# Kernel optimization log

Measured on AMD Instinct MI355X. Metric: run time of the kernel, lower is better.

## Reference

```python
import jax, jax.numpy as jnp
import numpy as np

D_MODEL = 1024
NUM_HEADS = 16
HEAD_DIM = D_MODEL // NUM_HEADS


def setup_inputs() -> dict:
    key = jax.random.key(0)
    ks = jax.random.split(key, 8)
    B, S = 4, 1024
    scale = 1.0 / np.sqrt(D_MODEL)
    return {
        "x": jax.random.normal(ks[0], (B, S, D_MODEL), jnp.float32),
        "tokens": jax.random.normal(ks[1], (B, 1, D_MODEL), jnp.float32),
        "Wq": jax.random.normal(ks[2], (D_MODEL, D_MODEL), jnp.float32) * scale,
        "bq": jnp.zeros((D_MODEL,), jnp.float32),
        "Wk": jax.random.normal(ks[3], (D_MODEL, D_MODEL), jnp.float32) * scale,
        "bk": jnp.zeros((D_MODEL,), jnp.float32),
        "Wv": jax.random.normal(ks[4], (D_MODEL, D_MODEL), jnp.float32) * scale,
        "bv": jnp.zeros((D_MODEL,), jnp.float32),
    }


def _split_heads(t):
    # [B, S, D] -> [B, H, S, hd]
    B, S, _ = t.shape
    return t.reshape(B, S, NUM_HEADS, HEAD_DIM).transpose(0, 2, 1, 3)


def reference(x, tokens, Wq, bq, Wk, bk, Wv, bv):
    # Projections (torch Linear: y = x @ W.T + b)
    Q = _split_heads(x @ Wq.T + bq)          # [B,H,S,hd]
    K = _split_heads(x @ Wk.T + bk)
    V = _split_heads(x @ Wv.T + bv)
    tQ = _split_heads(tokens @ Wq.T + bq)    # [B,H,1,hd] -> broadcast
    tK = _split_heads(tokens @ Wk.T + bk)
    cQ = Q + tQ
    cK = K + tK
    scores = jnp.einsum("bhqd,bhkd->bhqk", cQ, cK) / jnp.sqrt(jnp.float32(HEAD_DIM))
    attn = jax.nn.softmax(scores, axis=-1)
    out = jnp.einsum("bhqk,bhkd->bhqd", attn, V)  # [B,H,S,hd]
    B, H, S, hd = out.shape
    return out.transpose(0, 2, 1, 3).reshape(B, S, D_MODEL)
```

## Files before the change

kernel.cpp:

```cpp
#include <hip/hip_runtime.h>
#include <hip/hip_bf16.h>


typedef __bf16 bf16;
typedef __bf16 bf16x8 __attribute__((ext_vector_type(8)));
typedef float  f32x4  __attribute__((ext_vector_type(4)));

#define LOG2E 1.4426950408889634f

__device__ __forceinline__ void gll16(const void* g, void* l) {
  __builtin_amdgcn_global_load_lds(
      (const __attribute__((address_space(1))) unsigned int*)g,
      (__attribute__((address_space(3))) unsigned int*)l, 16, 0, 0);
}

__device__ __forceinline__ unsigned cvtpk(float a, float b) {
  unsigned r;
  asm("v_cvt_pk_bf16_f32 %0, %1, %2" : "=v"(r) : "v"(a), "v"(b));
  return r;
}

__global__ void prep_kernel(const float* __restrict__ x, const float* __restrict__ tok,
                            const float* __restrict__ wq, const float* __restrict__ wk,
                            const float* __restrict__ wv,
                            bf16* __restrict__ xb, bf16* __restrict__ xt,
                            bf16* __restrict__ wdst) {
  const int bid = blockIdx.x;
  if (bid < 2048) {
    const size_t e = ((size_t)bid * 256 + threadIdx.x) * 8;
    const int b = (int)(e >> 20);
    const int d = (int)(e & 1023);
    const float4 a0 = *(const float4*)(x + e);
    const float4 a1 = *(const float4*)(x + e + 4);
    const float4 t0 = *(const float4*)(tok + b * 1024 + d);
    const float4 t1 = *(const float4*)(tok + b * 1024 + d + 4);
    bf16x8 vb, vt;
    vb[0]=(bf16)a0.x; vb[1]=(bf16)a0.y; vb[2]=(bf16)a0.z; vb[3]=(bf16)a0.w;
    vb[4]=(bf16)a1.x; vb[5]=(bf16)a1.y; vb[6]=(bf16)a1.z; vb[7]=(bf16)a1.w;
    vt[0]=(bf16)(a0.x+t0.x); vt[1]=(bf16)(a0.y+t0.y); vt[2]=(bf16)(a0.z+t0.z); vt[3]=(bf16)(a0.w+t0.w);
    vt[4]=(bf16)(a1.x+t1.x); vt[5]=(bf16)(a1.y+t1.y); vt[6]=(bf16)(a1.z+t1.z); vt[7]=(bf16)(a1.w+t1.w);
    *(bf16x8*)(xb + e) = vb;
    *(bf16x8*)(xt + e) = vt;
  } else {
    const size_t e = ((size_t)(bid - 2048) * 256 + threadIdx.x) * 8;
    const float* src; size_t off;
    if (e < (size_t)(1u<<20))      { src = wq; off = e; }
    else if (e < (size_t)(2u<<20)) { src = wk; off = e - (1u<<20); }
    else                           { src = wv; off = e - (2u<<20); }
    const float4 a0 = *(const float4*)(src + off);
    const float4 a1 = *(const float4*)(src + off + 4);
    bf16x8 v;
    v[0]=(bf16)a0.x; v[1]=(bf16)a0.y; v[2]=(bf16)a0.z; v[3]=(bf16)a0.w;
    v[4]=(bf16)a1.x; v[5]=(bf16)a1.y; v[6]=(bf16)a1.z; v[7]=(bf16)a1.w;
    *(bf16x8*)(wdst + e) = v;
  }
}

__global__ __launch_bounds__(256, 3) void qkv_gemm_kernel(
    const bf16* __restrict__ xt, const bf16* __restrict__ xb,
    const bf16* __restrict__ wq, const bf16* __restrict__ wk, const bf16* __restrict__ wv,
    const float* __restrict__ bq, const float* __restrict__ bk, const float* __restrict__ bv,
    bf16* __restrict__ cq, bf16* __restrict__ ck, bf16* __restrict__ vt)
{
  __shared__ __align__(16) char LDSG[49152];
  char* As = LDSG;
  char* Bs = LDSG + 24576;
  const int t = threadIdx.x, w = t >> 6, l = t & 63, g = l >> 4, c = l & 15;
  const int wr = w >> 1, wc = w & 1;
  const int wgid = blockIdx.x;
  const int xcd = wgid & 7;
  const int p = wgid >> 3;
  const int z = p >> 5;
  const int q = p & 31;
  const bf16 *A, *B; const float* bias; bf16* outp;
  int tm, tn;
  if (z < 2) { tm = xcd * 4 + (q & 3); tn = q >> 2; }
  else       { tm = q >> 2; tn = xcd * 4 + (q & 3); }
  if (z == 0)      { A = xt; B = wq; bias = bq; outp = cq; }
  else if (z == 1) { A = xt; B = wk; bias = bk; outp = ck; }
  else             { A = wv; B = xb; bias = bv; outp = vt; }
  const int m0 = tm * 128, n0 = tn * 128;

  f32x4 acc[4][4] = {};

  const int u = (t & 7) ^ ((t >> 3) & 7);
  const size_t ssw = (size_t)(2 * (t >> 3) + (u >> 2)) * 2048 + (size_t)(u & 3) * 16;
  const char* aga = (const char*)A + (size_t)m0 * 2048 + ssw;
  const char* bga = (const char*)B + (size_t)n0 * 2048 + ssw;

#define GSTAGE(slot, kt)                                                 \
  {                                                                      \
    const size_t ko = (size_t)(kt) * 64;            \
    char* ad = As + (slot) * 8192 + t * 16;                              \
    char* bd = Bs + (slot) * 8192 + t * 16;                              \
    gll16(aga + ko,          ad);                                        \
    gll16(aga + ko + 131072, ad + 4096);             \
    gll16(bga + ko,          bd);                                        \
    gll16(bga + ko + 131072, bd + 4096);                                 \
  }

  GSTAGE(0, 0);
  GSTAGE(1, 1);
  int st = 2;
  int s  = 0;
  for (int kt = 0; kt < 32; ++kt) {
    if (kt < 30) {
      GSTAGE(st, kt + 2);
      asm volatile("s_waitcnt vmcnt(8)" ::: "memory");
    } else if (kt == 30) {
      asm volatile("s_waitcnt vmcnt(4)" ::: "memory");
    } else {
      asm volatile("s_waitcnt vmcnt(0)" ::: "memory");
    }
    __builtin_amdgcn_sched_barrier(0);
    __builtin_amdgcn_s_barrier();

    const char* Ab = As + s * 8192;
    const char* Bb = Bs + s * 8192;
    bf16x8 af[4], bfr[4];
#pragma unroll
    for (int mf = 0; mf < 4; ++mf) {
      const int mrow = wr * 64 + mf * 16 + c;
      af[mf] = *(const bf16x8*)(Ab + (mrow >> 1) * 128 +
                                (((((mrow & 1) << 2) + g) ^ ((mrow >> 1) & 7)) << 4));
    }
#pragma unroll
    for (int nf = 0; nf < 4; ++nf) {
      const int nrow = wc * 64 + nf * 16 + c;
      bfr[nf] = *(const bf16x8*)(Bb + (nrow >> 1) * 128 +
                                 (((((nrow & 1) << 2) + g) ^ ((nrow >> 1) & 7)) << 4));
    }
    __builtin_amdgcn_s_setprio(1);
#pragma unroll
    for (int mf = 0; mf < 4; ++mf)
#pragma unroll
      for (int nf = 0; nf < 4; ++nf)
        acc[mf][nf] = __builtin_amdgcn_mfma_f32_16x16x32_bf16(af[mf], bfr[nf], acc[mf][nf], 0, 0, 0);
    __builtin_amdgcn_s_setprio(0);
    __builtin_amdgcn_s_barrier();
    s  = (s  == 2) ? 0 : s + 1;
    st = (st == 2) ? 0 : st + 1;
  }
#undef GSTAGE

  if (z < 2) {
    const float sc = (z == 0) ? 0.125f * LOG2E : 1.0f;
#pragma unroll
    for (int mf = 0; mf < 4; ++mf)
#pragma unroll
      for (int nf = 0; nf < 4; ++nf) {
        const int n = n0 + wc * 64 + nf * 16 + c;
        const int h = n >> 6, d = n & 63;
        const float bsum = 2.0f * bias[n];
#pragma unroll
        for (int r = 0; r < 4; ++r) {
          const int m = m0 + wr * 64 + mf * 16 + g * 4 + r;
          const int b = m >> 10, s2 = m & 1023;
          outp[(((size_t)(b * 16 + h)) * 1024 + s2) * 64 + d] = (bf16)((acc[mf][nf][r] + bsum) * sc);
        }
      }
  } else {
#pragma unroll
    for (int mf = 0; mf < 4; ++mf)
#pragma unroll
      for (int nf = 0; nf < 4; ++nf) {
        const int n = n0 + wc * 64 + nf * 16 + c;
        const int b = n >> 10, s2 = n & 1023;
#pragma unroll
        for (int r = 0; r < 4; ++r) {
          const int m = m0 + wr * 64 + mf * 16 + g * 4 + r;
          const int h = m >> 6, d = m & 63;
          outp[(((size_t)(b * 16 + h)) * 64 + d) * 1024 + s2] = (bf16)(acc[mf][nf][r] + bias[m]);
        }
      }
  }
}

__global__ __launch_bounds__(256) void attn_kernel(
    const bf16* __restrict__ cq, const bf16* __restrict__ ck, const bf16* __restrict__ vt,
    float* __restrict__ out)
{
  __shared__ __align__(16) char LDS[32768];
  const int t = threadIdx.x, w = t >> 6, l = t & 63, g = l >> 4, c = l & 15;
  const int bh = blockIdx.y, qt = blockIdx.x;
  const int b = bh >> 4, h = bh & 15;
  const bf16* cqb = cq + (size_t)bh * 65536;
  const bf16* ckb = ck + (size_t)bh * 65536;
  const bf16* vtb = vt + (size_t)bh * 65536;
  const int q0 = qt * 64 + w * 16;

  bf16x8 qf[2];
#pragma unroll
  for (int kf = 0; kf < 2; ++kf)
    qf[kf] = *(const bf16x8*)(cqb + (size_t)(q0 + c) * 64 + kf * 32 + g * 8);

  f32x4 o[4] = {};
  float m = -INFINITY, lsum = 0.f;

  const int srow = t >> 3;
  const int sch  = (t & 7) ^ (srow & 7);
  const int kap = ((srow >> 4) & 1) * 32 + ((srow >> 2) & 3) * 8 + (srow & 3);
  const size_t ksrc1 = (size_t)kap * 128 + (size_t)sch * 16;
  const size_t ksrc2 = ksrc1 + 512;
  const size_t vsrc  = (size_t)srow * 2048 + (size_t)sch * 16;

#define STAGE(buf, t0)                                                   \
  {                                                                      \
    const char* kgb = (const char*)ckb + (size_t)(t0) * 128;             \
    const char* vgb = (const char*)vtb + (size_t)(t0) * 2;               \
    char* kd = LDS + (buf) * 8192 + w * 1024;                            \
    char* vd = LDS + 16384 + (buf) * 8192 + w * 1024;                    \
    gll16(kgb + ksrc1,        kd);                                       \
    gll16(kgb + ksrc2,        kd + 4096);           \
    gll16(vgb + vsrc,         vd);                                       \
    gll16(vgb + 65536 + vsrc, vd + 4096);             \
  }

  STAGE(0, 0);
  __syncthreads();
  int buf = 0;

  for (int t0 = 0; t0 < 1024; t0 += 64) {
    if (t0 + 64 < 1024) STAGE(buf ^ 1, t0 + 64);
    const char* Kb = LDS + buf * 8192;
    const char* Vb = LDS + 16384 + buf * 8192;

    f32x4 s[4] = {};
#pragma unroll
    for (int kf = 0; kf < 2; ++kf)
#pragma unroll
      for (int nf = 0; nf < 4; ++nf) {
        const int kr = nf * 16 + c;
        bf16x8 kb = *(const bf16x8*)(Kb + kr * 128 + (((kf * 4 + g) ^ (kr & 7)) << 4));
        s[nf] = __builtin_amdgcn_mfma_f32_16x16x32_bf16(kb, qf[kf], s[nf], 0, 0, 0);
      }

    float vmax = s[0][0];
#pragma unroll
    for (int nf = 0; nf < 4; ++nf)
#pragma unroll
      for (int r = 0; r < 4; ++r) vmax = fmaxf(vmax, s[nf][r]);
    vmax = fmaxf(vmax, __shfl_xor(vmax, 16, 64));
    vmax = fmaxf(vmax, __shfl_xor(vmax, 32, 64));
    if (!__all(vmax - m <= 8.0f)) {
      const float mnew = fmaxf(m, vmax);
      const float alpha = exp2f(m - mnew);
      m = mnew;
      lsum *= alpha;
#pragma unroll
      for (int nd = 0; nd < 4; ++nd) o[nd] *= alpha;
    }

    float p[4][4];
    float ps = 0.f;
#pragma unroll
    for (int nf = 0; nf < 4; ++nf)
#pragma unroll
      for (int r = 0; r < 4; ++r) {
        p[nf][r] = exp2f(s[nf][r] - m);
        ps += p[nf][r];
      }
    ps += __shfl_xor(ps, 16, 64);
    ps += __shfl_xor(ps, 32, 64);
    lsum += ps;

    union { unsigned u[4]; bf16x8 v; } pa0, pa1;
    pa0.u[0] = cvtpk(p[0][0], p[0][1]); pa0.u[1] = cvtpk(p[0][2], p[0][3]);
    pa0.u[2] = cvtpk(p[2][0], p[2][1]); pa0.u[3] = cvtpk(p[2][2], p[2][3]);
    pa1.u[0] = cvtpk(p[1][0], p[1][1]); pa1.u[1] = cvtpk(p[1][2], p[1][3]);
    pa1.u[2] = cvtpk(p[3][0], p[3][1]); pa1.u[3] = cvtpk(p[3][2], p[3][3]);

#pragma unroll
    for (int kf = 0; kf < 2; ++kf) {
      const bf16x8 pav = kf ? pa1.v : pa0.v;
#pragma unroll
      for (int nd = 0; nd < 4; ++nd) {
        const int vr = nd * 16 + c;
        bf16x8 vb = *(const bf16x8*)(Vb + vr * 128 + (((kf * 4 + g) ^ (vr & 7)) << 4));
        o[nd] = __builtin_amdgcn_mfma_f32_16x16x32_bf16(vb, pav, o[nd], 0, 0, 0);
      }
    }

    __syncthreads();
    buf ^= 1;
  }

#undef STAGE

  const float inv = 1.0f / lsum;
  {
    char* Ob = LDS;
    const int row = w * 16 + c;
#pragma unroll
    for (int nd = 0; nd < 4; ++nd) {
      f32x4 vo = o[nd] * inv;
      const int pch = (nd * 4 + g) ^ (row & 7);
      *(f32x4*)(Ob + row * 256 + (pch << 4)) = vo;
    }
  }
  __syncthreads();
  {
    const int rr = t >> 2;
    float* orow = out + ((size_t)(b * 1024 + qt * 64 + rr)) * 1024 + h * 64;
#pragma unroll
    for (int i = 0; i < 4; ++i) {
      const int ch = (t & 3) + i * 4;
      f32x4 v = *(const f32x4*)(LDS + rr * 256 + ((ch ^ (rr & 7)) << 4));
      *(f32x4*)(orow + ch * 4) = v;
    }
  }
}

extern "C" void kernel_launch(void* const* d_in, const int* in_sizes, int n_in,
                              void* d_out, int out_size, void* d_ws, size_t ws_size,
                              hipStream_t stream) {
  const float* x   = (const float*)d_in[0];
  const float* tok = (const float*)d_in[1];
  const float* Wq  = (const float*)d_in[2];
  const float* bq  = (const float*)d_in[3];
  const float* Wk  = (const float*)d_in[4];
  const float* bk  = (const float*)d_in[5];
  const float* Wv  = (const float*)d_in[6];
  const float* bv  = (const float*)d_in[7];
  float* out = (float*)d_out;
  char* ws = (char*)d_ws;
  bf16* xt  = (bf16*)(ws + (size_t)0);
  bf16* xb  = (bf16*)(ws + ((size_t)8  << 20));
  bf16* wqb = (bf16*)(ws + ((size_t)16 << 20));
  bf16* wkb = (bf16*)(ws + ((size_t)18 << 20));
  bf16* wvb = (bf16*)(ws + ((size_t)20 << 20));
  bf16* cqw = (bf16*)(ws + ((size_t)22 << 20));
  bf16* ckw = (bf16*)(ws + ((size_t)30 << 20));
  bf16* vtw = (bf16*)(ws + ((size_t)38 << 20));

  prep_kernel<<<dim3(3584), dim3(256), 0, stream>>>(x, tok, Wq, Wk, Wv, xb, xt, wqb);
  qkv_gemm_kernel<<<dim3(768), dim3(256), 0, stream>>>(
      xt, xb, wqb, wkb, wvb, bq, bk, bv, cqw, ckw, vtw);
  attn_kernel<<<dim3(16, 64), dim3(256), 0, stream>>>(cqw, ckw, vtw, out);
}
```

Baseline: 87.27 us.

## Use 512-thread attention blocks with 128 queries and triple-buffered K/V staging

```diff
diff --git a/kernel.cpp b/kernel.cpp
--- a/kernel.cpp
+++ b/kernel.cpp
@@ -90,11 +90,11 @@
 
 #define GSTAGE(slot, kt)                                                 \
   {                                                                      \
-    const size_t ko = (size_t)(kt) * 64;            \
+    const size_t ko = (size_t)(kt) * 64;                                 \
     char* ad = As + (slot) * 8192 + t * 16;                              \
     char* bd = Bs + (slot) * 8192 + t * 16;                              \
     gll16(aga + ko,          ad);                                        \
-    gll16(aga + ko + 131072, ad + 4096);             \
+    gll16(aga + ko + 131072, ad + 4096);                                 \
     gll16(bga + ko,          bd);                                        \
     gll16(bga + ko + 131072, bd + 4096);                                 \
   }
@@ -176,18 +176,18 @@
   }
 }
 
-__global__ __launch_bounds__(256) void attn_kernel(
+__global__ __launch_bounds__(512) void attn_kernel(
     const bf16* __restrict__ cq, const bf16* __restrict__ ck, const bf16* __restrict__ vt,
     float* __restrict__ out)
 {
-  __shared__ __align__(16) char LDS[32768];
+  __shared__ __align__(16) char LDS[49152];
   const int t = threadIdx.x, w = t >> 6, l = t & 63, g = l >> 4, c = l & 15;
   const int bh = blockIdx.y, qt = blockIdx.x;
   const int b = bh >> 4, h = bh & 15;
   const bf16* cqb = cq + (size_t)bh * 65536;
   const bf16* ckb = ck + (size_t)bh * 65536;
   const bf16* vtb = vt + (size_t)bh * 65536;
-  const int q0 = qt * 64 + w * 16;
+  const int q0 = qt * 128 + w * 16;
 
   bf16x8 qf[2];
 #pragma unroll
@@ -197,49 +197,54 @@
   f32x4 o[4] = {};
   float m = -INFINITY, lsum = 0.f;
 
-  const int srow = t >> 3;
-  const int sch  = (t & 7) ^ (srow & 7);
-  const int kap = ((srow >> 4) & 1) * 32 + ((srow >> 2) & 3) * 8 + (srow & 3);
-  const size_t ksrc1 = (size_t)kap * 128 + (size_t)sch * 16;
-  const size_t ksrc2 = ksrc1 + 512;
-  const size_t vsrc  = (size_t)srow * 2048 + (size_t)sch * 16;
-
-#define STAGE(buf, t0)                                                   \
+  const int r_ = t >> 3;
+  const int sch = (t & 7) ^ (r_ & 7);
+  const int kap = ((r_ >> 4) & 1) * 32 + ((r_ >> 2) & 3) * 8 + ((r_ >> 5) & 1) * 4 + (r_ & 3);
+  const size_t ksrc = (size_t)kap * 128 + (size_t)sch * 16;
+  const size_t vsrc = (size_t)r_ * 2048 + (size_t)sch * 16;
+
+#define STAGE(slot, idx)                                                 \
   {                                                                      \
-    const char* kgb = (const char*)ckb + (size_t)(t0) * 128;             \
-    const char* vgb = (const char*)vtb + (size_t)(t0) * 2;               \
-    char* kd = LDS + (buf) * 8192 + w * 1024;                            \
-    char* vd = LDS + 16384 + (buf) * 8192 + w * 1024;                    \
-    gll16(kgb + ksrc1,        kd);                                       \
-    gll16(kgb + ksrc2,        kd + 4096);           \
-    gll16(vgb + vsrc,         vd);                                       \
-    gll16(vgb + 65536 + vsrc, vd + 4096);             \
+    const char* kgb = (const char*)ckb + (size_t)(idx) * 8192;           \
+    const char* vgb = (const char*)vtb + (size_t)(idx) * 128;            \
+    gll16(kgb + ksrc, LDS + (slot) * 8192 + t * 16);                     \
+    gll16(vgb + vsrc, LDS + 24576 + (slot) * 8192 + t * 16);             \
   }
 
   STAGE(0, 0);
-  __syncthreads();
-  int buf = 0;
-
-  for (int t0 = 0; t0 < 1024; t0 += 64) {
-    if (t0 + 64 < 1024) STAGE(buf ^ 1, t0 + 64);
-    const char* Kb = LDS + buf * 8192;
-    const char* Vb = LDS + 16384 + buf * 8192;
-
-    f32x4 s[4] = {};
+  STAGE(1, 1);
+  int st = 2;
+  int s  = 0;
+  for (int idx = 0; idx < 16; ++idx) {
+    if (idx < 14) {
+      STAGE(st, idx + 2);
+      asm volatile("s_waitcnt vmcnt(4)" ::: "memory");
+    } else if (idx == 14) {
+      asm volatile("s_waitcnt vmcnt(2)" ::: "memory");
+    } else {
+      asm volatile("s_waitcnt vmcnt(0)" ::: "memory");
+    }
+    __builtin_amdgcn_sched_barrier(0);
+    __builtin_amdgcn_s_barrier();
+
+    const char* Kb = LDS + s * 8192;
+    const char* Vb = LDS + 24576 + s * 8192;
+
+    f32x4 sv[4] = {};
 #pragma unroll
     for (int kf = 0; kf < 2; ++kf)
 #pragma unroll
       for (int nf = 0; nf < 4; ++nf) {
         const int kr = nf * 16 + c;
         bf16x8 kb = *(const bf16x8*)(Kb + kr * 128 + (((kf * 4 + g) ^ (kr & 7)) << 4));
-        s[nf] = __builtin_amdgcn_mfma_f32_16x16x32_bf16(kb, qf[kf], s[nf], 0, 0, 0);
-      }
-
-    float vmax = s[0][0];
+        sv[nf] = __builtin_amdgcn_mfma_f32_16x16x32_bf16(kb, qf[kf], sv[nf], 0, 0, 0);
+      }
+
+    float vmax = sv[0][0];
 #pragma unroll
     for (int nf = 0; nf < 4; ++nf)
 #pragma unroll
-      for (int r = 0; r < 4; ++r) vmax = fmaxf(vmax, s[nf][r]);
+      for (int r = 0; r < 4; ++r) vmax = fmaxf(vmax, sv[nf][r]);
     vmax = fmaxf(vmax, __shfl_xor(vmax, 16, 64));
     vmax = fmaxf(vmax, __shfl_xor(vmax, 32, 64));
     if (!__all(vmax - m <= 8.0f)) {
@@ -257,7 +262,7 @@
     for (int nf = 0; nf < 4; ++nf)
 #pragma unroll
       for (int r = 0; r < 4; ++r) {
-        p[nf][r] = exp2f(s[nf][r] - m);
+        p[nf][r] = exp2f(sv[nf][r] - m);
         ps += p[nf][r];
       }
     ps += __shfl_xor(ps, 16, 64);
@@ -281,10 +286,10 @@
       }
     }
 
-    __syncthreads();
-    buf ^= 1;
-  }
-
+    __builtin_amdgcn_s_barrier();
+    s  = (s  == 2) ? 0 : s + 1;
+    st = (st == 2) ? 0 : st + 1;
+  }
 #undef STAGE
 
   const float inv = 1.0f / lsum;
@@ -301,7 +306,7 @@
   __syncthreads();
   {
     const int rr = t >> 2;
-    float* orow = out + ((size_t)(b * 1024 + qt * 64 + rr)) * 1024 + h * 64;
+    float* orow = out + ((size_t)(b * 1024 + qt * 128 + rr)) * 1024 + h * 64;
 #pragma unroll
     for (int i = 0; i < 4; ++i) {
       const int ch = (t & 3) + i * 4;
@@ -336,5 +341,5 @@
   prep_kernel<<<dim3(3584), dim3(256), 0, stream>>>(x, tok, Wq, Wk, Wv, xb, xt, wqb);
   qkv_gemm_kernel<<<dim3(768), dim3(256), 0, stream>>>(
       xt, xb, wqb, wkb, wvb, bq, bk, bv, cqw, ckw, vtw);
-  attn_kernel<<<dim3(16, 64), dim3(256), 0, stream>>>(cqw, ckw, vtw, out);
-}
+  attn_kernel<<<dim3(8, 64), dim3(512), 0, stream>>>(cqw, ckw, vtw, out);
+}
```

Measured after the change: 82.61 us. -5.3%, faster.
